# Performance work log

Measured on AMD Instinct MI355X. Metric: run time of the kernel, lower is better.

Reference implementation:

```python
import jax, jax.numpy as jnp
import numpy as np

N = 100000   # num_nodes
E = 1600000  # num_edges (avg degree 16)
D = 64       # embed_channels
C = 16       # num_classes
EPSILON = 0.1  # AntiSymmetricConv step size (PyG default)
GAMMA = 0.1    # AntiSymmetricConv diffusion strength (PyG default)


def setup_inputs() -> dict:
    key = jax.random.key(0)
    ks = jax.random.split(key, 9)
    s = 1.0 / np.sqrt(D)
    return {
        "edge_index": jax.random.randint(ks[0], (2, E), 0, N, dtype=jnp.int32),
        "embed_w": jax.random.normal(ks[1], (N, D), dtype=jnp.float32) * 0.1,
        "W_rel": jax.random.normal(ks[2], (D, D), dtype=jnp.float32) * s,   # GraphConv lin_rel weight
        "b_rel": jax.random.normal(ks[3], (D,), dtype=jnp.float32) * s,     # GraphConv lin_rel bias
        "W_root": jax.random.normal(ks[4], (D, D), dtype=jnp.float32) * s,  # GraphConv lin_root weight (no bias)
        "W_anti": jax.random.normal(ks[5], (D, D), dtype=jnp.float32) * s,  # AntiSymmetricConv W
        "b_anti": jax.random.normal(ks[6], (D,), dtype=jnp.float32) * s,    # AntiSymmetricConv bias
        "W_lin": jax.random.normal(ks[7], (C, D), dtype=jnp.float32) * s,   # lin2 weight
        "b_lin": jax.random.normal(ks[8], (C,), dtype=jnp.float32) * s,     # lin2 bias
    }


def reference(edge_index, embed_w, W_rel, b_rel, W_root, W_anti, b_anti, W_lin, b_lin):
    x = embed_w  # [N, D] node features = embedding table
    src, dst = edge_index[0], edge_index[1]
    # phi = GraphConv with 'add' aggregation: lin_rel(sum_j x_j) + lin_root(x)
    agg = jax.ops.segment_sum(x[src], dst, num_segments=N)  # [N, D] sparse gather+scatter-add
    h = agg @ W_rel.T + b_rel + x @ W_root.T
    # antisymmetric weight: W - W^T - gamma * I
    aW = W_anti - W_anti.T - GAMMA * jnp.eye(D, dtype=x.dtype)
    h = x @ aW.T + h + b_anti
    h = jnp.tanh(h)                       # default act of AntiSymmetricConv
    x = x + EPSILON * h                   # single iteration (num_iters=1 default)
    # dropout p=0.0 -> identity
    out = jax.nn.sigmoid(x @ W_lin.T + b_lin)  # [N, C]
    return out
```

## Files before the change

kernel.cpp:

```cpp
#include <hip/hip_runtime.h>

#define DD 64
#define CC 16
#define EPSILON 0.1f
#define GAMMA 0.1f
#define BSH 6
#define BSZ 64
#define CAP 1280
#define MAXBK 2048
#define PAD 65
#define PADW 65
#define CSH 10
#define MAXNC 128
#define CAPC 20480
#define L1CHUNK 2048
#define L1THR 512
#define NSLICE 8
#define SRTSZ 2560

typedef float v2f __attribute__((ext_vector_type(2)));

__global__ __launch_bounds__(L1THR) void bin_coarse_conv(
        const int* __restrict__ ei, int* __restrict__ gcntc,
        unsigned* __restrict__ binned_c, int E,
        const float* __restrict__ x, unsigned* __restrict__ x_q, int N) {
    __shared__ unsigned sorted[SRTSZ];
    __shared__ unsigned char bkt[SRTSZ];
    __shared__ int hist[MAXNC], ph[MAXNC], base[MAXNC], cur[MAXNC], gbase[MAXNC];
    __shared__ int mtot;
    const int t = threadIdx.x;
    if (t < MAXNC) hist[t] = 0;
    __syncthreads();
    const int e0 = blockIdx.x * L1CHUNK;
    unsigned ent[L1CHUNK / L1THR];
    int cbk[L1CHUNK / L1THR];
#pragma unroll
    for (int i = 0; i < L1CHUNK / L1THR; ++i) {
        int e = e0 + t + L1THR * i;
        cbk[i] = -1;
        if (e < E) {
            int src = ei[e], dst = ei[E + e];
            cbk[i] = dst >> CSH;
            ent[i] = (unsigned)src | ((unsigned)(dst & ((1 << CSH) - 1)) << 17);
            atomicAdd(&hist[cbk[i]], 1);
        }
    }
    __syncthreads();
    if (t < MAXNC) { ph[t] = (hist[t] + 3) & ~3; cur[t] = ph[t]; }
    __syncthreads();
    for (int off = 1; off < MAXNC; off <<= 1) {
        int v = 0;
        if (t < MAXNC && t >= off) v = cur[t - off];
        __syncthreads();
        if (t < MAXNC) cur[t] += v;
        __syncthreads();
    }
    if (t < MAXNC) {
        base[t] = cur[t] - ph[t];
        if (t == MAXNC - 1) mtot = cur[t];
        cur[t] = base[t];
    }
    __syncthreads();
#pragma unroll
    for (int i = 0; i < L1CHUNK / L1THR; ++i)
        if (cbk[i] >= 0) {
            int pos = atomicAdd(&cur[cbk[i]], 1);
            sorted[pos] = ent[i];
            bkt[pos] = (unsigned char)cbk[i];
        }
    __syncthreads();
    if (t < MAXNC) {
        int b0 = base[t] + hist[t], b1 = base[t] + ph[t];
        for (int p = b0; p < b1; ++p) {
            sorted[p] = 0xFFFFFFFFu;
            bkt[p] = (unsigned char)t;
        }
        gbase[t] = ph[t] ? atomicAdd(&gcntc[t], ph[t]) : 0;
    }
    __syncthreads();
    const int m = mtot;
    for (int j4 = 4 * t; j4 < m; j4 += 4 * L1THR) {
        int cb = bkt[j4];
        int gp = gbase[cb] + (j4 - base[cb]);
        if (gp + 4 <= CAPC) {
            uint4 v = *(const uint4*)&sorted[j4];
            *(uint4*)&binned_c[(size_t)cb * CAPC + gp] = v;
        }
    }
    const float4* x4 = (const float4*)x;
    const int M = N * (DD / 4);
    const int G = gridDim.x * L1THR;
    for (int i = blockIdx.x * L1THR + t; i < M; i += G) {
        float4 a = x4[i];
        int r = __builtin_amdgcn_cvt_pk_fp8_f32(a.x, a.y, 0, false);
        r = __builtin_amdgcn_cvt_pk_fp8_f32(a.z, a.w, r, true);
        x_q[i] = (unsigned)r;
    }
}

__global__ __launch_bounds__(256) void bin_fine_w(
        const int* __restrict__ gcntc, const unsigned* __restrict__ binned_c,
        int* __restrict__ gcnt, unsigned* __restrict__ binned,
        const float* __restrict__ Wrel, const float* __restrict__ Wroot,
        const float* __restrict__ Wanti, const float* __restrict__ brel,
        const float* __restrict__ banti,
        float* __restrict__ B_g, float* __restrict__ bc) {
    const int t = threadIdx.x;
    if (blockIdx.x == gridDim.x - 1) {
        for (int idx = t; idx < 128 * 64; idx += 256) {
            int k = idx >> 6, d = idx & 63;
            float v;
            if (k < 64) {
                v = Wrel[d * 64 + k];
            } else {
                int j = k - 64;
                v = Wroot[d * 64 + j] + Wanti[d * 64 + j] - Wanti[j * 64 + d];
                if (d == j) v -= GAMMA;
            }
            B_g[idx] = v;
        }
        if (t < 64) bc[t] = brel[t] + banti[t];
        return;
    }
    __shared__ int hist[16];
    __shared__ int hbase[16];
    const int c = blockIdx.x >> 3, s = blockIdx.x & (NSLICE - 1);
    int cnt = gcntc[c];
    if (cnt > CAPC) cnt = CAPC;
    const int per = (cnt + NSLICE - 1) / NSLICE;
    const int i0 = s * per;
    int i1 = i0 + per;
    if (i1 > cnt) i1 = cnt;
    if (t < 16) hist[t] = 0;
    __syncthreads();
    const unsigned* bcp = binned_c + (size_t)c * CAPC;
    unsigned ent[10];
#pragma unroll
    for (int j = 0; j < 10; ++j) {
        int i = i0 + t + j * 256;
        ent[j] = (i < i1) ? bcp[i] : 0xFFFFFFFFu;
        if (ent[j] != 0xFFFFFFFFu) atomicAdd(&hist[ent[j] >> (17 + BSH)], 1);
    }
    __syncthreads();
    if (t < 16) {
        hbase[t] = hist[t] ? atomicAdd(&gcnt[c * 16 + t], hist[t]) : 0;
        hist[t] = 0;
    }
    __syncthreads();
#pragma unroll
    for (int j = 0; j < 10; ++j) {
        if (ent[j] != 0xFFFFFFFFu) {
            unsigned dstc = ent[j] >> 17;
            int f = dstc >> BSH;
            int pos = hbase[f] + atomicAdd(&hist[f], 1);
            if (pos < CAP)
                binned[(size_t)(c * 16 + f) * CAP + pos] =
                    (ent[j] & 0x1FFFF) | ((dstc & (BSZ - 1)) << 17);
        }
    }
}

__global__ __launch_bounds__(512, 8) void mega(
        const float* __restrict__ x, const unsigned* __restrict__ x_q,
        const int* __restrict__ gcnt, const unsigned* __restrict__ binned,
        const float* __restrict__ B_g, const float* __restrict__ bc,
        const float* __restrict__ Wlin, const float* __restrict__ blin,
        float* __restrict__ out, int N) {
    __shared__ float R0[BSZ * PAD];
    __shared__ float wl_sh[CC * PADW];
    __shared__ int csr[CAP];
    __shared__ int deg[BSZ], offs[BSZ], cur[BSZ];

    const int t = threadIdx.x;
    const int b = blockIdx.x;
    const int nb0 = b << BSH;
    int cnt = gcnt[b];
    if (cnt > CAP) cnt = CAP;
    const unsigned* bl = binned + (size_t)b * CAP;

#pragma unroll
    for (int i = 0; i < 2; ++i) {
        int idx = t + 512 * i;
        wl_sh[(idx >> 6) * PADW + (idx & 63)] = Wlin[idx];
    }
    if (t < BSZ) deg[t] = 0;
    __syncthreads();
    for (int i = t; i < cnt; i += 512) atomicAdd(&deg[bl[i] >> 17], 1);
    __syncthreads();
    if (t < BSZ) offs[t] = deg[t];
    __syncthreads();
    for (int off = 1; off < BSZ; off <<= 1) {
        int v = 0;
        if (t < BSZ && t >= off) v = offs[t - off];
        __syncthreads();
        if (t < BSZ) offs[t] += v;
        __syncthreads();
    }
    if (t < BSZ) {
        int ex = offs[t] - deg[t];
        offs[t] = ex;
        cur[t] = ex;
    }
    __syncthreads();
    for (int i = t; i < cnt; i += 512) {
        unsigned en = bl[i];
        int pos = atomicAdd(&cur[en >> 17], 1);
        csr[pos] = (int)(en & 0x1FFFF);
    }
    __syncthreads();

    {
        const int g = t >> 3, q = t & 7;
        const uint2* xq2 = (const uint2*)x_q;
        const int i0 = offs[g], dc = deg[g];
        float a0[8], a1[8];
#pragma unroll
        for (int r = 0; r < 8; ++r) { a0[r] = 0.f; a1[r] = 0.f; }
        int i = 0;
        for (; i + 2 <= dc; i += 2) {
            int s0 = csr[i0 + i], s1 = csr[i0 + i + 1];
            uint2 v0 = xq2[s0 * 8 + q];
            uint2 v1 = xq2[s1 * 8 + q];
            v2f f;
            f = __builtin_amdgcn_cvt_pk_f32_fp8(v0.x, false); a0[0] += f.x; a0[1] += f.y;
            f = __builtin_amdgcn_cvt_pk_f32_fp8(v0.x, true);  a0[2] += f.x; a0[3] += f.y;
            f = __builtin_amdgcn_cvt_pk_f32_fp8(v0.y, false); a0[4] += f.x; a0[5] += f.y;
            f = __builtin_amdgcn_cvt_pk_f32_fp8(v0.y, true);  a0[6] += f.x; a0[7] += f.y;
            f = __builtin_amdgcn_cvt_pk_f32_fp8(v1.x, false); a1[0] += f.x; a1[1] += f.y;
            f = __builtin_amdgcn_cvt_pk_f32_fp8(v1.x, true);  a1[2] += f.x; a1[3] += f.y;
            f = __builtin_amdgcn_cvt_pk_f32_fp8(v1.y, false); a1[4] += f.x; a1[5] += f.y;
            f = __builtin_amdgcn_cvt_pk_f32_fp8(v1.y, true);  a1[6] += f.x; a1[7] += f.y;
        }
        if (i < dc) {
            int s0 = csr[i0 + i];
            uint2 v0 = xq2[s0 * 8 + q];
            v2f f;
            f = __builtin_amdgcn_cvt_pk_f32_fp8(v0.x, false); a0[0] += f.x; a0[1] += f.y;
            f = __builtin_amdgcn_cvt_pk_f32_fp8(v0.x, true);  a0[2] += f.x; a0[3] += f.y;
            f = __builtin_amdgcn_cvt_pk_f32_fp8(v0.y, false); a0[4] += f.x; a0[5] += f.y;
            f = __builtin_amdgcn_cvt_pk_f32_fp8(v0.y, true);  a0[6] += f.x; a0[7] += f.y;
        }
        float* row = &R0[g * PAD + 8 * q];
#pragma unroll
        for (int r = 0; r < 8; ++r) row[r] = a0[r] + a1[r];
    }
    __syncthreads();

    const int nl = t & 63;
    const int dg = __builtin_amdgcn_readfirstlane(t >> 6);
    float acc[8];
#pragma unroll
    for (int j = 0; j < 8; ++j) acc[j] = 0.f;
#pragma unroll 8
    for (int k = 0; k < DD; ++k) {
        float a = R0[nl * PAD + k];
        const float* Bk = &B_g[k * DD + dg * 8];
#pragma unroll
        for (int j = 0; j < 8; ++j) acc[j] = fmaf(a, Bk[j], acc[j]);
    }
    __syncthreads();

    {
        int nn = N - nb0;
        if (nn > BSZ) nn = BSZ;
        const float4* x4 = (const float4*)x;
        for (int idx = t; idx < nn * 16; idx += 512) {
            float4 v = x4[nb0 * 16 + idx];
            float* row = &R0[(idx >> 4) * PAD + (idx & 15) * 4];
            row[0] = v.x; row[1] = v.y; row[2] = v.z; row[3] = v.w;
        }
    }
    __syncthreads();

#pragma unroll 8
    for (int k = 0; k < DD; ++k) {
        float a = R0[nl * PAD + k];
        const float* Bk = &B_g[(DD + k) * DD + dg * 8];
#pragma unroll
        for (int j = 0; j < 8; ++j) acc[j] = fmaf(a, Bk[j], acc[j]);
    }

#pragma unroll
    for (int j = 0; j < 8; ++j) {
        int d = dg * 8 + j;
        float h = acc[j] + bc[d];
        float e2 = __expf(2.0f * h);
        float th = 1.0f - 2.0f / (e2 + 1.0f);
        acc[j] = R0[nl * PAD + d] + EPSILON * th;
    }
    __syncthreads();
#pragma unroll
    for (int j = 0; j < 8; ++j) R0[nl * PAD + dg * 8 + j] = acc[j];
    __syncthreads();

    {
        const int g = t >> 3, q = t & 7;
        const int n = nb0 + g;
        if (n < N) {
            float p0 = blin[2 * q], p1 = blin[2 * q + 1];
#pragma unroll 8
            for (int d = 0; d < DD; ++d) {
                float xv = R0[g * PAD + d];
                p0 = fmaf(xv, wl_sh[(2 * q) * PADW + d], p0);
                p1 = fmaf(xv, wl_sh[(2 * q + 1) * PADW + d], p1);
            }
            float2 o;
            o.x = 1.0f / (1.0f + __expf(-p0));
            o.y = 1.0f / (1.0f + __expf(-p1));
            *(float2*)(out + (size_t)n * CC + 2 * q) = o;
        }
    }
}

extern "C" void kernel_launch(void* const* d_in, const int* in_sizes, int n_in,
                              void* d_out, int out_size, void* d_ws, size_t ws_size,
                              hipStream_t stream) {
    const int*   ei    = (const int*)d_in[0];
    const float* x     = (const float*)d_in[1];
    const float* Wrel  = (const float*)d_in[2];
    const float* brel  = (const float*)d_in[3];
    const float* Wroot = (const float*)d_in[4];
    const float* Wanti = (const float*)d_in[5];
    const float* banti = (const float*)d_in[6];
    const float* Wlin  = (const float*)d_in[7];
    const float* blin  = (const float*)d_in[8];
    float* out = (float*)d_out;

    const int E = in_sizes[0] / 2;
    const int N = in_sizes[1] / DD;
    const int NC = (N + (1 << CSH) - 1) >> CSH;

    unsigned* x_q = (unsigned*)d_ws;
    unsigned* binned_c = x_q + (size_t)N * (DD / 4);
    unsigned* binned = binned_c + (size_t)MAXNC * CAPC;
    int*   gcntc = (int*)(binned + (size_t)MAXBK * CAP);
    int*   gcnt  = gcntc + MAXNC;
    float* B_g   = (float*)(gcnt + MAXBK);
    float* bc    = B_g + 128 * 64;

    hipMemsetAsync(gcntc, 0, (MAXNC + MAXBK) * sizeof(int), stream);
    bin_coarse_conv<<<(E + L1CHUNK - 1) / L1CHUNK, L1THR, 0, stream>>>(
        ei, gcntc, binned_c, E, x, x_q, N);
    bin_fine_w<<<NC * NSLICE + 1, 256, 0, stream>>>(
        gcntc, binned_c, gcnt, binned, Wrel, Wroot, Wanti, brel, banti, B_g, bc);
    mega<<<NC * 16, 512, 0, stream>>>(x, x_q, gcnt, binned, B_g, bc, Wlin, blin, out, N);
}
```

Measured before the change: 173.6 us.

## Pad coarse counters, move weight prep to first kernel, unroll gather by 8

Pads the coarse bin counters to one counter per 16 ints, which spreads the global atomics so they no longer share cache lines. Moves the combined-weight and bias construction from a dedicated extra block in the fine-binning kernel into block 0 of the coarse kernel. Unrolls the fp8 neighbor gather loop to 8 loads per iteration with a single accumulator set, so more memory loads are in flight at once. The trade-offs are higher register pressure, extra work on block 0 of the coarse kernel, and a slightly larger counter region to memset.

```diff
diff --git a/kernel.cpp b/kernel.cpp
--- a/kernel.cpp
+++ b/kernel.cpp
@@ -12,6 +12,7 @@
 #define PADW 65
 #define CSH 10
 #define MAXNC 128
+#define CPAD 16
 #define CAPC 20480
 #define L1CHUNK 2048
 #define L1THR 512
@@ -23,7 +24,11 @@
 __global__ __launch_bounds__(L1THR) void bin_coarse_conv(
         const int* __restrict__ ei, int* __restrict__ gcntc,
         unsigned* __restrict__ binned_c, int E,
-        const float* __restrict__ x, unsigned* __restrict__ x_q, int N) {
+        const float* __restrict__ x, unsigned* __restrict__ x_q, int N,
+        const float* __restrict__ Wrel, const float* __restrict__ Wroot,
+        const float* __restrict__ Wanti, const float* __restrict__ brel,
+        const float* __restrict__ banti,
+        float* __restrict__ B_g, float* __restrict__ bc) {
     __shared__ unsigned sorted[SRTSZ];
     __shared__ unsigned char bkt[SRTSZ];
     __shared__ int hist[MAXNC], ph[MAXNC], base[MAXNC], cur[MAXNC], gbase[MAXNC];
@@ -75,7 +80,7 @@
             sorted[p] = 0xFFFFFFFFu;
             bkt[p] = (unsigned char)t;
         }
-        gbase[t] = ph[t] ? atomicAdd(&gcntc[t], ph[t]) : 0;
+        gbase[t] = ph[t] ? atomicAdd(&gcntc[t * CPAD], ph[t]) : 0;
     }
     __syncthreads();
     const int m = mtot;
@@ -87,27 +92,8 @@
             *(uint4*)&binned_c[(size_t)cb * CAPC + gp] = v;
         }
     }
-    const float4* x4 = (const float4*)x;
-    const int M = N * (DD / 4);
-    const int G = gridDim.x * L1THR;
-    for (int i = blockIdx.x * L1THR + t; i < M; i += G) {
-        float4 a = x4[i];
-        int r = __builtin_amdgcn_cvt_pk_fp8_f32(a.x, a.y, 0, false);
-        r = __builtin_amdgcn_cvt_pk_fp8_f32(a.z, a.w, r, true);
-        x_q[i] = (unsigned)r;
-    }
-}
-
-__global__ __launch_bounds__(256) void bin_fine_w(
-        const int* __restrict__ gcntc, const unsigned* __restrict__ binned_c,
-        int* __restrict__ gcnt, unsigned* __restrict__ binned,
-        const float* __restrict__ Wrel, const float* __restrict__ Wroot,
-        const float* __restrict__ Wanti, const float* __restrict__ brel,
-        const float* __restrict__ banti,
-        float* __restrict__ B_g, float* __restrict__ bc) {
-    const int t = threadIdx.x;
-    if (blockIdx.x == gridDim.x - 1) {
-        for (int idx = t; idx < 128 * 64; idx += 256) {
+    if (blockIdx.x == 0) {
+        for (int idx = t; idx < 128 * 64; idx += L1THR) {
             int k = idx >> 6, d = idx & 63;
             float v;
             if (k < 64) {
@@ -120,12 +106,26 @@
             B_g[idx] = v;
         }
         if (t < 64) bc[t] = brel[t] + banti[t];
-        return;
-    }
+    }
+    const float4* x4 = (const float4*)x;
+    const int M = N * (DD / 4);
+    const int G = gridDim.x * L1THR;
+    for (int i = blockIdx.x * L1THR + t; i < M; i += G) {
+        float4 a = x4[i];
+        int r = __builtin_amdgcn_cvt_pk_fp8_f32(a.x, a.y, 0, false);
+        r = __builtin_amdgcn_cvt_pk_fp8_f32(a.z, a.w, r, true);
+        x_q[i] = (unsigned)r;
+    }
+}
+
+__global__ __launch_bounds__(256) void bin_fine(
+        const int* __restrict__ gcntc, const unsigned* __restrict__ binned_c,
+        int* __restrict__ gcnt, unsigned* __restrict__ binned) {
     __shared__ int hist[16];
     __shared__ int hbase[16];
+    const int t = threadIdx.x;
     const int c = blockIdx.x >> 3, s = blockIdx.x & (NSLICE - 1);
-    int cnt = gcntc[c];
+    int cnt = gcntc[c * CPAD];
     if (cnt > CAPC) cnt = CAPC;
     const int per = (cnt + NSLICE - 1) / NSLICE;
     const int i0 = s * per;
@@ -213,36 +213,42 @@
         const int g = t >> 3, q = t & 7;
         const uint2* xq2 = (const uint2*)x_q;
         const int i0 = offs[g], dc = deg[g];
-        float a0[8], a1[8];
-#pragma unroll
-        for (int r = 0; r < 8; ++r) { a0[r] = 0.f; a1[r] = 0.f; }
+        float a[8];
+#pragma unroll
+        for (int r = 0; r < 8; ++r) a[r] = 0.f;
         int i = 0;
-        for (; i + 2 <= dc; i += 2) {
-            int s0 = csr[i0 + i], s1 = csr[i0 + i + 1];
+        for (; i + 8 <= dc; i += 8) {
+            int s0 = csr[i0 + i + 0], s1 = csr[i0 + i + 1];
+            int s2 = csr[i0 + i + 2], s3 = csr[i0 + i + 3];
+            int s4 = csr[i0 + i + 4], s5 = csr[i0 + i + 5];
+            int s6 = csr[i0 + i + 6], s7 = csr[i0 + i + 7];
             uint2 v0 = xq2[s0 * 8 + q];
             uint2 v1 = xq2[s1 * 8 + q];
+            uint2 v2 = xq2[s2 * 8 + q];
+            uint2 v3 = xq2[s3 * 8 + q];
+            uint2 v4 = xq2[s4 * 8 + q];
+            uint2 v5 = xq2[s5 * 8 + q];
+            uint2 v6 = xq2[s6 * 8 + q];
+            uint2 v7 = xq2[s7 * 8 + q];
             v2f f;
-            f = __builtin_amdgcn_cvt_pk_f32_fp8(v0.x, false); a0[0] += f.x; a0[1] += f.y;
-            f = __builtin_amdgcn_cvt_pk_f32_fp8(v0.x, true);  a0[2] += f.x; a0[3] += f.y;
-            f = __builtin_amdgcn_cvt_pk_f32_fp8(v0.y, false); a0[4] += f.x; a0[5] += f.y;
-            f = __builtin_amdgcn_cvt_pk_f32_fp8(v0.y, true);  a0[6] += f.x; a0[7] += f.y;
-            f = __builtin_amdgcn_cvt_pk_f32_fp8(v1.x, false); a1[0] += f.x; a1[1] += f.y;
-            f = __builtin_amdgcn_cvt_pk_f32_fp8(v1.x, true);  a1[2] += f.x; a1[3] += f.y;
-            f = __builtin_amdgcn_cvt_pk_f32_fp8(v1.y, false); a1[4] += f.x; a1[5] += f.y;
-            f = __builtin_amdgcn_cvt_pk_f32_fp8(v1.y, true);  a1[6] += f.x; a1[7] += f.y;
-        }
-        if (i < dc) {
+#define ACC8(v)                                                               \
+            f = __builtin_amdgcn_cvt_pk_f32_fp8((v).x, false); a[0] += f.x; a[1] += f.y; \
+            f = __builtin_amdgcn_cvt_pk_f32_fp8((v).x, true);  a[2] += f.x; a[3] += f.y; \
+            f = __builtin_amdgcn_cvt_pk_f32_fp8((v).y, false); a[4] += f.x; a[5] += f.y; \
+            f = __builtin_amdgcn_cvt_pk_f32_fp8((v).y, true);  a[6] += f.x; a[7] += f.y;
+            ACC8(v0); ACC8(v1); ACC8(v2); ACC8(v3);
+            ACC8(v4); ACC8(v5); ACC8(v6); ACC8(v7);
+        }
+        for (; i < dc; ++i) {
             int s0 = csr[i0 + i];
             uint2 v0 = xq2[s0 * 8 + q];
             v2f f;
-            f = __builtin_amdgcn_cvt_pk_f32_fp8(v0.x, false); a0[0] += f.x; a0[1] += f.y;
-            f = __builtin_amdgcn_cvt_pk_f32_fp8(v0.x, true);  a0[2] += f.x; a0[3] += f.y;
-            f = __builtin_amdgcn_cvt_pk_f32_fp8(v0.y, false); a0[4] += f.x; a0[5] += f.y;
-            f = __builtin_amdgcn_cvt_pk_f32_fp8(v0.y, true);  a0[6] += f.x; a0[7] += f.y;
+            ACC8(v0);
+#undef ACC8
         }
         float* row = &R0[g * PAD + 8 * q];
 #pragma unroll
-        for (int r = 0; r < 8; ++r) row[r] = a0[r] + a1[r];
+        for (int r = 0; r < 8; ++r) row[r] = a[r];
     }
     __syncthreads();
 
@@ -334,14 +340,15 @@
     unsigned* binned_c = x_q + (size_t)N * (DD / 4);
     unsigned* binned = binned_c + (size_t)MAXNC * CAPC;
     int*   gcntc = (int*)(binned + (size_t)MAXBK * CAP);
-    int*   gcnt  = gcntc + MAXNC;
+    int*   gcnt  = gcntc + MAXNC * CPAD;
     float* B_g   = (float*)(gcnt + MAXBK);
     float* bc    = B_g + 128 * 64;
 
-    hipMemsetAsync(gcntc, 0, (MAXNC + MAXBK) * sizeof(int), stream);
+    hipMemsetAsync(gcntc, 0, (MAXNC * CPAD + MAXBK) * sizeof(int), stream);
     bin_coarse_conv<<<(E + L1CHUNK - 1) / L1CHUNK, L1THR, 0, stream>>>(
-        ei, gcntc, binned_c, E, x, x_q, N);
-    bin_fine_w<<<NC * NSLICE + 1, 256, 0, stream>>>(
-        gcntc, binned_c, gcnt, binned, Wrel, Wroot, Wanti, brel, banti, B_g, bc);
-    mega<<<NC * 16, 512, 0, stream>>>(x, x_q, gcnt, binned, B_g, bc, Wlin, blin, out, N);
+        ei, gcntc, binned_c, E, x, x_q, N,
+        Wrel, Wroot, Wanti, brel, banti, B_g, bc);
+    bin_fine<<<NC * NSLICE, 256, 0, stream>>>(gcntc, binned_c, gcnt, binned);
+    mega<<<NC * 16, 512, 0, stream>>>(x, x_q, gcnt, binned, B_g, bc, Wlin, blin,
+                                      out, N);
 }
```

Result: no change. 176.1 us (+1.5%).
